# Performance work log

Measured on AMD Instinct MI355X. Metric: run time of the kernel, lower is better.

## Reference

```python
import jax, jax.numpy as jnp
import numpy as np

B, N, C = 4, 1024, 768
H = 12
HD = C // H  # 64
SCALE = HD ** -0.5


def setup_inputs() -> dict:
    key = jax.random.key(0)
    ks = jax.random.split(key, 8)
    s = lambda fan: 1.0 / np.sqrt(fan)
    return {
        "inputs": jax.random.normal(ks[0], (B, N, C), jnp.float32),
        "w_qkv": jax.random.normal(ks[1], (C, 3 * C), jnp.float32) * s(C),
        "w_l": jax.random.normal(ks[2], (H, H), jnp.float32) * s(H),
        "b_l": jnp.zeros((H,), jnp.float32),
        "w_w": jax.random.normal(ks[3], (H, H), jnp.float32) * s(H),
        "b_w": jnp.zeros((H,), jnp.float32),
        "w_proj": jax.random.normal(ks[4], (C, C), jnp.float32) * s(C),
        "b_proj": jnp.zeros((C,), jnp.float32),
    }


def reference(inputs, w_qkv, w_l, b_l, w_w, b_w, w_proj, b_proj):
    b, n, c = inputs.shape
    qkv = inputs @ w_qkv                      # (B,N,3C), no bias (use_att_bias=False)
    qkv = qkv.reshape(b, n, 3, H, HD)
    qkv = jnp.transpose(qkv, (2, 0, 3, 1, 4))  # (3,B,H,N,HD)
    q = qkv[0] * SCALE
    k = qkv[1]
    v = qkv[2]
    att = jnp.einsum("bhqd,bhkd->bhqk", q, k)            # (B,H,N,N)
    # pre-softmax talking-heads mix over head axis
    att = jnp.einsum("bhqk,hg->bgqk", att, w_l) + b_l[None, :, None, None]
    att = jax.nn.softmax(att, axis=-1)
    # post-softmax talking-heads mix
    att = jnp.einsum("bhqk,hg->bgqk", att, w_w) + b_w[None, :, None, None]
    x = jnp.einsum("bhqk,bhkd->bqhd", att, v).reshape(b, n, c)
    return x @ w_proj + b_proj
```

## Files before the change

### kernel.cpp

```cpp
#include <hip/hip_runtime.h>


#define Bsz   4
#define Nseq  1024
#define Cdim  768
#define Hn    12
#define HDim  64

typedef __attribute__((ext_vector_type(4))) float    f32x4;
typedef __attribute__((ext_vector_type(8))) _Float16 f16x8;
typedef __attribute__((ext_vector_type(4))) _Float16 f16x4;

#define MFMA_F16(A, B, C) __builtin_amdgcn_mfma_f32_16x16x32_f16(A, B, C, 0, 0, 0)

__global__ __launch_bounds__(256) void cvt_f32_f16(
    const float* __restrict__ in, _Float16* __restrict__ out)
{
  const size_t i = (size_t)(blockIdx.x * 256 + threadIdx.x) * 4;
  float4 v = *(const float4*)(in + i);
  f16x4 o;
  o[0] = (_Float16)v.x; o[1] = (_Float16)v.y;
  o[2] = (_Float16)v.z; o[3] = (_Float16)v.w;
  *(f16x4*)(out + i) = o;
}

__global__ __launch_bounds__(256) void transpose_cvt(
    const float* __restrict__ in, _Float16* __restrict__ out, int R, int C)
{
  __shared__ float T[64][65];
  const int c0 = blockIdx.x * 64, r0 = blockIdx.y * 64;
  const int lr = threadIdx.x >> 4, lc = (threadIdx.x & 15) * 4;
#pragma unroll
  for (int i = 0; i < 4; ++i) {
    float4 v = *(const float4*)(in + (size_t)(r0 + lr + i*16) * C + c0 + lc);
    T[lr+i*16][lc+0] = v.x; T[lr+i*16][lc+1] = v.y;
    T[lr+i*16][lc+2] = v.z; T[lr+i*16][lc+3] = v.w;
  }
  __syncthreads();
#pragma unroll
  for (int i = 0; i < 4; ++i) {
    const int orow = lr + i*16;
    f16x4 o;
#pragma unroll
    for (int j = 0; j < 4; ++j) o[j] = (_Float16)T[lc+j][orow];
    *(f16x4*)(out + (size_t)(c0 + orow) * R + r0 + lc) = o;
  }
}

__global__ __launch_bounds__(256, 2) void gemm_f16(
    const _Float16* __restrict__ A, const _Float16* __restrict__ Bt,
    const float* __restrict__ bias, _Float16* __restrict__ C16,
    float* __restrict__ C32, int M, int N, int K)
{
  __shared__ _Float16 sA[2][4][512];
  __shared__ _Float16 sB[2][4][512];
  const int tid = threadIdx.x;
  const int w = tid >> 6, lane = tid & 63;
  const int m0 = blockIdx.y * 128, n0 = blockIdx.x * 128;
  const int frow = lane & 15, fk8 = lane >> 4;

  f32x4 acc[4][4];
#pragma unroll
  for (int i = 0; i < 4; ++i)
#pragma unroll
    for (int j = 0; j < 4; ++j) acc[i][j] = (f32x4)0.f;

  const _Float16* gsrc = (w < 2)
      ? A  + (size_t)(m0 + w*64 + frow) * K + fk8 * 8
      : Bt + (size_t)(n0 + (w - 2)*64 + frow) * K + fk8 * 8;

  for (int kt = 0; kt < K; kt += 32) {
    f16x8 st[4];
#pragma unroll
    for (int j = 0; j < 4; ++j)
      st[j] = *(const f16x8*)(gsrc + kt + (size_t)j * 16 * K);
    __syncthreads();
    if (w < 2) {
#pragma unroll
      for (int j = 0; j < 4; ++j) *(f16x8*)&sA[w][j][lane*8] = st[j];
    } else {
#pragma unroll
      for (int j = 0; j < 4; ++j) *(f16x8*)&sB[w-2][j][lane*8] = st[j];
    }
    __syncthreads();
    f16x8 af[4], bf[4];
#pragma unroll
    for (int mi = 0; mi < 4; ++mi) af[mi] = *(const f16x8*)&sA[w & 1][mi][lane*8];
#pragma unroll
    for (int ni = 0; ni < 4; ++ni) bf[ni] = *(const f16x8*)&sB[w >> 1][ni][lane*8];
#pragma unroll
    for (int mi = 0; mi < 4; ++mi)
#pragma unroll
      for (int ni = 0; ni < 4; ++ni)
        acc[mi][ni] = MFMA_F16(af[mi], bf[ni], acc[mi][ni]);
  }

  const int m0w = m0 + (w & 1) * 64, n0w = n0 + (w >> 1) * 64;
#pragma unroll
  for (int mi = 0; mi < 4; ++mi)
#pragma unroll
    for (int ni = 0; ni < 4; ++ni) {
      const int n = n0w + ni*16 + (lane & 15);
#pragma unroll
      for (int r = 0; r < 4; ++r) {
        const int m = m0w + mi*16 + (lane >> 4)*4 + r;
        if (C16) C16[(size_t)m * N + n] = (_Float16)acc[mi][ni][r];
        else     C32[(size_t)m * N + n] = acc[mi][ni][r] + bias[n];
      }
    }
}

__global__ __launch_bounds__(256, 2) void gemm_s16(
    const _Float16* __restrict__ qkv16, _Float16* __restrict__ S)
{
  __shared__ _Float16 sA[2][4][512];
  __shared__ _Float16 sB[2][4][512];
  const int tid = threadIdx.x;
  const int w = tid >> 6, lane = tid & 63;
  const int m0 = blockIdx.y * 128, n0 = blockIdx.x * 128;
  const int frow = lane & 15, fk8 = lane >> 4;
  const int bh = blockIdx.z;
  const int b = bh / Hn, h = bh % Hn;

  const _Float16* Abase = qkv16 + (size_t)(b * Nseq) * (3*Cdim) + h * HDim;
  const _Float16* Bbase = Abase + Cdim;

  f32x4 acc[4][4];
#pragma unroll
  for (int i = 0; i < 4; ++i)
#pragma unroll
    for (int j = 0; j < 4; ++j) acc[i][j] = (f32x4)0.f;

  const _Float16* gsrc = (w < 2)
      ? Abase + (size_t)(m0 + w*64 + frow) * (3*Cdim) + fk8 * 8
      : Bbase + (size_t)(n0 + (w - 2)*64 + frow) * (3*Cdim) + fk8 * 8;

#pragma unroll
  for (int kt = 0; kt < HDim; kt += 32) {
    f16x8 st[4];
#pragma unroll
    for (int j = 0; j < 4; ++j)
      st[j] = *(const f16x8*)(gsrc + kt + (size_t)j * 16 * (3*Cdim));
    __syncthreads();
    if (w < 2) {
#pragma unroll
      for (int j = 0; j < 4; ++j) *(f16x8*)&sA[w][j][lane*8] = st[j];
    } else {
#pragma unroll
      for (int j = 0; j < 4; ++j) *(f16x8*)&sB[w-2][j][lane*8] = st[j];
    }
    __syncthreads();
    f16x8 af[4], bf[4];
#pragma unroll
    for (int mi = 0; mi < 4; ++mi) af[mi] = *(const f16x8*)&sA[w & 1][mi][lane*8];
#pragma unroll
    for (int ni = 0; ni < 4; ++ni) bf[ni] = *(const f16x8*)&sB[w >> 1][ni][lane*8];
#pragma unroll
    for (int mi = 0; mi < 4; ++mi)
#pragma unroll
      for (int ni = 0; ni < 4; ++ni)
        acc[mi][ni] = MFMA_F16(af[mi], bf[ni], acc[mi][ni]);
  }

  _Float16* out = S + ((size_t)bh << 20);
  const int m0w = m0 + (w & 1) * 64, n0w = n0 + (w >> 1) * 64;
#pragma unroll
  for (int mi = 0; mi < 4; ++mi)
#pragma unroll
    for (int ni = 0; ni < 4; ++ni) {
      const int n = n0w + ni*16 + (lane & 15);
#pragma unroll
      for (int r = 0; r < 4; ++r) {
        const int m = m0w + mi*16 + (lane >> 4)*4 + r;
        out[(size_t)m * Nseq + n] = (_Float16)acc[mi][ni][r];
      }
    }
}

__global__ __launch_bounds__(256) void mixexp_k(
    _Float16* __restrict__ S, const float* __restrict__ w_l)
{
  __shared__ __attribute__((aligned(16))) float wl_s[144];
  __shared__ float dred[4][12];
  __shared__ float dfin[2][12];
  const int tid = threadIdx.x;
  if (tid < 144) wl_s[tid] = w_l[tid] * 0.125f;
  __syncthreads();

  const int b   = blockIdx.x >> 9;
  const int qp  = blockIdx.x & 511;
  const int ql  = tid >> 7;
  const int q   = qp * 2 + ql;
  const int ks  = (tid & 127) * 8;
  _Float16* base = S + ((size_t)(b*Hn) << 20) + ((size_t)q << 10) + ks;

  f16x8 sv[12];
#pragma unroll
  for (int h = 0; h < 12; ++h) sv[h] = *(const f16x8*)(base + ((size_t)h << 20));

  float dacc[12];
#pragma unroll
  for (int g = 0; g < 12; ++g) dacc[g] = 0.f;
  f16x8 pv[12];

#pragma unroll
  for (int kk = 0; kk < 8; ++kk) {
    float L[12];
#pragma unroll
    for (int g = 0; g < 12; ++g) L[g] = 0.f;
#pragma unroll
    for (int h = 0; h < 12; ++h) {
      const float s = (float)sv[h][kk];
      const f32x4 w0 = *(const f32x4*)&wl_s[h*12];
      const f32x4 w1 = *(const f32x4*)&wl_s[h*12+4];
      const f32x4 w2 = *(const f32x4*)&wl_s[h*12+8];
#pragma unroll
      for (int j = 0; j < 4; ++j) {
        L[j]   = fmaf(s, w0[j], L[j]);
        L[4+j] = fmaf(s, w1[j], L[4+j]);
        L[8+j] = fmaf(s, w2[j], L[8+j]);
      }
    }
#pragma unroll
    for (int g = 0; g < 12; ++g) {
      const _Float16 p16 = (_Float16)__expf(L[g] - 6.0f);
      pv[g][kk] = p16;
      dacc[g] += (float)p16;
    }
  }

  const int w = tid >> 6;
#pragma unroll
  for (int g = 0; g < 12; ++g) {
    float v = dacc[g];
    v += __shfl_xor(v, 1, 64);
    v += __shfl_xor(v, 2, 64);
    v += __shfl_xor(v, 4, 64);
    v += __shfl_xor(v, 8, 64);
    v += __shfl_xor(v, 16, 64);
    v += __shfl_xor(v, 32, 64);
    dacc[g] = v;
  }
  if ((tid & 63) == 0) {
#pragma unroll
    for (int g = 0; g < 12; ++g) dred[w][g] = dacc[g];
  }
  __syncthreads();
  if (tid < 24) {
    const int qi = tid / 12, g = tid % 12;
    dfin[qi][g] = 1.0f / (dred[qi*2][g] + dred[qi*2+1][g]);
  }
  __syncthreads();

#pragma unroll
  for (int g = 0; g < 12; ++g) {
    const float df = dfin[ql][g];
    f16x8 t = pv[g];
#pragma unroll
    for (int kk = 0; kk < 8; ++kk) t[kk] = (_Float16)((float)t[kk] * df);
    *(f16x8*)(base + ((size_t)g << 20)) = t;
  }
}

__global__ __launch_bounds__(256) void prep_v(
    const _Float16* __restrict__ qkv16, _Float16* __restrict__ Vt)
{
  __shared__ float vt[64][65];
  const int id = blockIdx.x;
  const int nt = id & 15;
  const int h  = (id >> 4) % Hn;
  const int b  = id / (16 * Hn);
  const int n0 = nt * 64;
  const int tid = threadIdx.x;
  const int row = tid >> 2;
  const int c0  = (tid & 3) * 16;

  const _Float16* src = qkv16 + (size_t)(b*Nseq + n0 + row) * (3*Cdim) + 2*Cdim + h*HDim + c0;
  f16x8 v0 = *(const f16x8*)src;
  f16x8 v1 = *(const f16x8*)(src + 8);
#pragma unroll
  for (int j = 0; j < 8; ++j) {
    vt[c0+j][row]   = (float)v0[j];
    vt[c0+8+j][row] = (float)v1[j];
  }
  __syncthreads();
  f16x8 o0, o1;
#pragma unroll
  for (int j = 0; j < 8; ++j) {
    o0[j] = (_Float16)vt[row][c0+j];
    o1[j] = (_Float16)vt[row][c0+8+j];
  }
  _Float16* dst = Vt + (size_t)((b*Hn + h)*HDim + row) * Nseq + n0 + c0;
  *(f16x8*)dst = o0;
  *(f16x8*)(dst + 8) = o1;
}

__global__ __launch_bounds__(256, 3) void pvmix2_k(
    const _Float16* __restrict__ P, const _Float16* __restrict__ Vt,
    const float* __restrict__ w_w, const float* __restrict__ b_w,
    float* __restrict__ x32)
{
  __shared__ _Float16 P_s[12][16][72];
  __shared__ __attribute__((aligned(16))) float ww_s[144];
  __shared__ float bw_s[12];

  const int tid = threadIdx.x;
  const int w = tid >> 6, lane = tid & 63;
  const int col = lane & 15, grp = lane >> 4;
  const int kq = blockIdx.x & 3;
  const int qt = (blockIdx.x >> 2) & 63;
  const int b  = blockIdx.x >> 8;
  const int q0 = qt << 4;

  if (tid < 144) ww_s[tid] = w_w[tid];
  if (tid < 12)  bw_s[tid] = b_w[tid];
  __syncthreads();

  f32x4 Y[12];
#pragma unroll
  for (int g2 = 0; g2 < 12; ++g2) Y[g2] = (f32x4)0.f;

  const int kk4 = (w*4 + grp) * 4;
  const _Float16* pb0 = P + ((size_t)(b*Hn) << 20) + ((size_t)(q0 + col) << 10);

  for (int c = kq*4; c < kq*4 + 4; ++c) {
    const int k0 = c * 64;
    float pf[12][4];
#pragma unroll
    for (int g = 0; g < 12; ++g) {
      const f16x4 t = *(const f16x4*)(pb0 + ((size_t)g << 20) + k0 + kk4);
#pragma unroll
      for (int j = 0; j < 4; ++j) pf[g][j] = (float)t[j];
    }
    __syncthreads();
#pragma unroll
    for (int g2 = 0; g2 < 12; ++g2) {
      float a0 = bw_s[g2], a1 = a0, a2 = a0, a3 = a0;
#pragma unroll
      for (int g = 0; g < 12; ++g) {
        const float wv = ww_s[g*12 + g2];
        a0 = fmaf(pf[g][0], wv, a0);
        a1 = fmaf(pf[g][1], wv, a1);
        a2 = fmaf(pf[g][2], wv, a2);
        a3 = fmaf(pf[g][3], wv, a3);
      }
      f16x4 o;
      o[0] = (_Float16)a0; o[1] = (_Float16)a1;
      o[2] = (_Float16)a2; o[3] = (_Float16)a3;
      *(f16x4*)&P_s[g2][col][kk4] = o;
    }
    __syncthreads();
#pragma unroll
    for (int g2 = 0; g2 < 12; ++g2) {
      f16x8 a0 = *(const f16x8*)&P_s[g2][col][grp*8];
      f16x8 a1 = *(const f16x8*)&P_s[g2][col][32 + grp*8];
      const _Float16* vb = Vt + (size_t)((b*Hn + g2)*HDim + w*16 + col) * Nseq
                           + k0 + grp*8;
      f16x8 v0 = *(const f16x8*)vb;
      f16x8 v1 = *(const f16x8*)(vb + 32);
      Y[g2] = MFMA_F16(a0, v0, Y[g2]);
      Y[g2] = MFMA_F16(a1, v1, Y[g2]);
    }
  }

#pragma unroll
  for (int g2 = 0; g2 < 12; ++g2)
#pragma unroll
    for (int r = 0; r < 4; ++r)
      atomicAdd(&x32[(size_t)(b*Nseq + q0 + grp*4 + r) * Cdim + g2*HDim + w*16 + col],
                Y[g2][r]);
}

__global__ __launch_bounds__(256, 2) void dsum_k(
    const _Float16* __restrict__ qkv16, const float* __restrict__ w_l,
    float* __restrict__ dpart)
{
  __shared__ __attribute__((aligned(16))) float wl_s[144];
  __shared__ float dred[4][16][12];
  const int tid = threadIdx.x;
  const int w = tid >> 6, lane = tid & 63;
  const int col = lane & 15, grp = lane >> 4;
  const int ch = blockIdx.x & 7;
  const int qt = (blockIdx.x >> 3) & 63;
  const int b  = blockIdx.x >> 9;
  const int q0 = qt << 4;

  if (tid < 144) wl_s[tid] = w_l[tid] * 0.125f;

  f16x8 qf[12][2];
  {
    const _Float16* qrow = qkv16 + (size_t)(b*Nseq + q0 + col) * (3*Cdim) + grp*8;
#pragma unroll
    for (int h = 0; h < 12; ++h) {
      qf[h][0] = *(const f16x8*)(qrow + h*HDim);
      qf[h][1] = *(const f16x8*)(qrow + h*HDim + 32);
    }
  }
  __syncthreads();

  float dacc[4][12];
#pragma unroll
  for (int r = 0; r < 4; ++r)
#pragma unroll
    for (int g = 0; g < 12; ++g) dacc[r][g] = 0.f;

#pragma unroll
  for (int kg = 0; kg < 2; ++kg) {
    const int key = ch*128 + kg*64 + w*16 + col;
    const _Float16* krow = qkv16 + (size_t)(b*Nseq + key) * (3*Cdim) + Cdim + grp*8;
    f32x4 S[12];
#pragma unroll
    for (int h = 0; h < 12; ++h) {
      f16x8 b0 = *(const f16x8*)(krow + h*HDim);
      f16x8 b1 = *(const f16x8*)(krow + h*HDim + 32);
      f32x4 s = (f32x4)0.f;
      s = MFMA_F16(qf[h][0], b0, s);
      S[h] = MFMA_F16(qf[h][1], b1, s);
    }
#pragma unroll
    for (int r = 0; r < 4; ++r) {
      float L[12];
#pragma unroll
      for (int g = 0; g < 12; ++g) L[g] = 0.f;
#pragma unroll
      for (int h = 0; h < 12; ++h) {
        const float s = S[h][r];
        const f32x4 w0 = *(const f32x4*)&wl_s[h*12];
        const f32x4 w1 = *(const f32x4*)&wl_s[h*12+4];
        const f32x4 w2 = *(const f32x4*)&wl_s[h*12+8];
#pragma unroll
        for (int j = 0; j < 4; ++j) {
          L[j]   = fmaf(s, w0[j], L[j]);
          L[4+j] = fmaf(s, w1[j], L[4+j]);
          L[8+j] = fmaf(s, w2[j], L[8+j]);
        }
      }
#pragma unroll
      for (int g = 0; g < 12; ++g) dacc[r][g] += __expf(L[g] - 6.0f);
    }
  }
#pragma unroll
  for (int r = 0; r < 4; ++r)
#pragma unroll
    for (int g = 0; g < 12; ++g) {
      float v = dacc[r][g];
      v += __shfl_xor(v, 1, 64);
      v += __shfl_xor(v, 2, 64);
      v += __shfl_xor(v, 4, 64);
      v += __shfl_xor(v, 8, 64);
      dacc[r][g] = v;
    }
  if (col == 0) {
#pragma unroll
    for (int r = 0; r < 4; ++r)
#pragma unroll
      for (int g = 0; g < 12; ++g) dred[w][grp*4+r][g] = dacc[r][g];
  }
  __syncthreads();
  if (tid < 192) {
    const int q = tid / 12, g = tid % 12;
    const float s = dred[0][q][g] + dred[1][q][g] + dred[2][q][g] + dred[3][q][g];
    dpart[((size_t)((b*Hn + g)*Nseq) + q0 + q) * 8 + ch] = s;
  }
}

__global__ __launch_bounds__(256) void dinv_k(
    const float* __restrict__ dpart, float* __restrict__ dinv)
{
  const int i = blockIdx.x * 256 + threadIdx.x;
  const float* p = dpart + (size_t)i * 8;
  f32x4 a = *(const f32x4*)p;
  f32x4 c = *(const f32x4*)(p + 4);
  dinv[i] = 1.0f / (a[0]+a[1]+a[2]+a[3]+c[0]+c[1]+c[2]+c[3]);
}

__global__ __launch_bounds__(256, 2) void pvmix_k(
    const _Float16* __restrict__ qkv16, const _Float16* __restrict__ Vt,
    const float* __restrict__ dinv,
    const float* __restrict__ w_l, const float* __restrict__ w_w,
    const float* __restrict__ b_w, float* __restrict__ x32)
{
  __shared__ _Float16 P_s[12][16][72];
  __shared__ float dinv_s[16][12];
  __shared__ __attribute__((aligned(16))) float wl_s[144];
  __shared__ __attribute__((aligned(16))) float ww_s[144];
  __shared__ float bw_s[12];

  const int tid = threadIdx.x;
  const int w = tid >> 6, lane = tid & 63;
  const int col = lane & 15, grp = lane >> 4;
  const int kh = blockIdx.x & 1;
  const int qt = (blockIdx.x >> 1) & 63;
  const int b  = blockIdx.x >> 7;
  const int q0 = qt << 4;

  if (tid < 144) { wl_s[tid] = w_l[tid] * 0.125f; ww_s[tid] = w_w[tid]; }
  if (tid < 12)  bw_s[tid] = b_w[tid];
  if (tid < 192) {
    const int q = tid / 12, g = tid % 12;
    dinv_s[q][g] = dinv[(size_t)((b*Hn + g)*Nseq) + q0 + q];
  }

  f16x8 qf[12][2];
  {
    const _Float16* qrow = qkv16 + (size_t)(b*Nseq + q0 + col) * (3*Cdim) + grp*8;
#pragma unroll
    for (int h = 0; h < 12; ++h) {
      qf[h][0] = *(const f16x8*)(qrow + h*HDim);
      qf[h][1] = *(const f16x8*)(qrow + h*HDim + 32);
    }
  }
  __syncthreads();

  f32x4 Y[12];
#pragma unroll
  for (int g2 = 0; g2 < 12; ++g2) Y[g2] = (f32x4)0.f;

  for (int c = kh*8; c < kh*8 + 8; ++c) {
    const int k0 = c * 64;
    const _Float16* krow = qkv16 + (size_t)(b*Nseq + k0 + w*16 + col) * (3*Cdim)
                           + Cdim + grp*8;
    f32x4 S[12];
#pragma unroll
    for (int h = 0; h < 12; ++h) {
      f16x8 b0 = *(const f16x8*)(krow + h*HDim);
      f16x8 b1 = *(const f16x8*)(krow + h*HDim + 32);
      f32x4 s = (f32x4)0.f;
      s = MFMA_F16(qf[h][0], b0, s);
      S[h] = MFMA_F16(qf[h][1], b1, s);
    }
    __syncthreads();
#pragma unroll
    for (int r = 0; r < 4; ++r) {
      const int q = grp*4 + r;
      float L[12];
#pragma unroll
      for (int g = 0; g < 12; ++g) L[g] = 0.f;
#pragma unroll
      for (int h = 0; h < 12; ++h) {
        const float s = S[h][r];
        const f32x4 w0 = *(const f32x4*)&wl_s[h*12];
        const f32x4 w1 = *(const f32x4*)&wl_s[h*12+4];
        const f32x4 w2 = *(const f32x4*)&wl_s[h*12+8];
#pragma unroll
        for (int j = 0; j < 4; ++j) {
          L[j]   = fmaf(s, w0[j], L[j]);
          L[4+j] = fmaf(s, w1[j], L[4+j]);
          L[8+j] = fmaf(s, w2[j], L[8+j]);
        }
      }
      float att2[12];
#pragma unroll
      for (int g2 = 0; g2 < 12; ++g2) att2[g2] = bw_s[g2];
#pragma unroll
      for (int g = 0; g < 12; ++g) {
        const float pr = __expf(L[g] - 6.0f) * dinv_s[q][g];
        const f32x4 w0 = *(const f32x4*)&ww_s[g*12];
        const f32x4 w1 = *(const f32x4*)&ww_s[g*12+4];
        const f32x4 w2 = *(const f32x4*)&ww_s[g*12+8];
#pragma unroll
        for (int j = 0; j < 4; ++j) {
          att2[j]   = fmaf(pr, w0[j], att2[j]);
          att2[4+j] = fmaf(pr, w1[j], att2[4+j]);
          att2[8+j] = fmaf(pr, w2[j], att2[8+j]);
        }
      }
#pragma unroll
      for (int g2 = 0; g2 < 12; ++g2)
        P_s[g2][q][w*16 + col] = (_Float16)att2[g2];
    }
    __syncthreads();
#pragma unroll
    for (int g2 = 0; g2 < 12; ++g2) {
      f16x8 a0 = *(const f16x8*)&P_s[g2][col][grp*8];
      f16x8 a1 = *(const f16x8*)&P_s[g2][col][32 + grp*8];
      const _Float16* vb = Vt + (size_t)((b*Hn + g2)*HDim + w*16 + col) * Nseq
                           + k0 + grp*8;
      f16x8 v0 = *(const f16x8*)vb;
      f16x8 v1 = *(const f16x8*)(vb + 32);
      Y[g2] = MFMA_F16(a0, v0, Y[g2]);
      Y[g2] = MFMA_F16(a1, v1, Y[g2]);
    }
  }

#pragma unroll
  for (int g2 = 0; g2 < 12; ++g2)
#pragma unroll
    for (int r = 0; r < 4; ++r)
      atomicAdd(&x32[(size_t)(b*Nseq + q0 + grp*4 + r) * Cdim + g2*HDim + w*16 + col],
                Y[g2][r]);
}

extern "C" void kernel_launch(void* const* d_in, const int* in_sizes, int n_in,
                              void* d_out, int out_size, void* d_ws, size_t ws_size,
                              hipStream_t stream) {
  (void)in_sizes; (void)n_in; (void)out_size;
  const float* inputs = (const float*)d_in[0];
  const float* w_qkv  = (const float*)d_in[1];
  const float* w_l    = (const float*)d_in[2];
  const float* w_w    = (const float*)d_in[4];
  const float* b_w    = (const float*)d_in[5];
  const float* w_proj = (const float*)d_in[6];
  const float* b_proj = (const float*)d_in[7];
  float* out = (float*)d_out;

  const int M = Bsz * Nseq;
  char* ws = (char*)d_ws;
  _Float16* A16   = (_Float16*)ws;
  _Float16* BtQKV = A16   + (size_t)M * Cdim;
  _Float16* BtPrj = BtQKV + (size_t)(3*Cdim) * Cdim;
  _Float16* qkv16 = BtPrj + (size_t)Cdim * Cdim;
  _Float16* Vt    = qkv16 + (size_t)M * 3 * Cdim;
  _Float16* x16   = Vt    + (size_t)M * Cdim;
  float*    dpart = (float*)(x16 + (size_t)M * Cdim);
  float*    dinv  = dpart + (size_t)Bsz*Hn*Nseq*8;
  float*    x32   = dinv  + (size_t)Bsz*Hn*Nseq;
  _Float16* S     = (_Float16*)(x32 + (size_t)M * Cdim);

  const size_t NEED = 42467328ull + 14352384ull + 100663296ull;

  cvt_f32_f16<<<dim3((M * Cdim) / 1024), 256, 0, stream>>>(inputs, A16);
  transpose_cvt<<<dim3((3*Cdim)/64, Cdim/64), 256, 0, stream>>>(w_qkv, BtQKV, Cdim, 3*Cdim);
  transpose_cvt<<<dim3(Cdim/64, Cdim/64), 256, 0, stream>>>(w_proj, BtPrj, Cdim, Cdim);

  gemm_f16<<<dim3((3*Cdim)/128, M/128), 256, 0, stream>>>(
      A16, BtQKV, nullptr, qkv16, nullptr, M, 3*Cdim, Cdim);

  prep_v<<<dim3(Bsz*Hn*16), 256, 0, stream>>>(qkv16, Vt);

  if (ws_size >= NEED) {
    gemm_s16<<<dim3(Nseq/128, Nseq/128, Bsz*Hn), 256, 0, stream>>>(qkv16, S);
    mixexp_k<<<dim3(Bsz*Nseq/2), 256, 0, stream>>>(S, w_l);
    hipMemsetAsync(x32, 0, (size_t)M*Cdim*sizeof(float), stream);
    pvmix2_k<<<dim3(Bsz*64*4), 256, 0, stream>>>(S, Vt, w_w, b_w, x32);
  } else {
    dsum_k<<<dim3(Bsz*64*8), 256, 0, stream>>>(qkv16, w_l, dpart);
    dinv_k<<<dim3(Bsz*Hn*Nseq/256), 256, 0, stream>>>(dpart, dinv);
    hipMemsetAsync(x32, 0, (size_t)M*Cdim*sizeof(float), stream);
    pvmix_k<<<dim3(Bsz*64*2), 256, 0, stream>>>(
        qkv16, Vt, dinv, w_l, w_w, b_w, x32);
  }

  cvt_f32_f16<<<dim3((M * Cdim) / 1024), 256, 0, stream>>>(x32, x16);

  gemm_f16<<<dim3(Cdim/128, M/128), 256, 0, stream>>>(
      x16, BtPrj, b_proj, nullptr, out, M, Cdim, Cdim);
}
```

Measured before the change: 330.8 us.

## Fuse post-softmax head mix into exp kernel and use plain PV GEMM

The post-softmax talking-heads mix (w_w, b_w) moves into the softmax normalisation kernel, which now writes fully mixed probabilities back to S. The P·V step then becomes a plain per-head GEMM writing fp16 straight into x16. This removes the split-K fp32 atomics, the x32 memset and the fp32-to-fp16 conversion pass. In exchange the exp kernel does more ALU work per element, and the new GEMM has a small N-tile (64) that uses only three of its four waves for loads.

Measured after the change: 288.4 us. -12.8%, faster.

```diff
diff --git a/kernel.cpp b/kernel.cpp
--- a/kernel.cpp
+++ b/kernel.cpp
@@ -177,14 +177,18 @@
     }
 }
 
-__global__ __launch_bounds__(256) void mixexp_k(
-    _Float16* __restrict__ S, const float* __restrict__ w_l)
+__global__ __launch_bounds__(256) void mixexp2_k(
+    _Float16* __restrict__ S, const float* __restrict__ w_l,
+    const float* __restrict__ w_w, const float* __restrict__ b_w)
 {
   __shared__ __attribute__((aligned(16))) float wl_s[144];
+  __shared__ __attribute__((aligned(16))) float ww_s[144];
+  __shared__ float bw_s[12];
   __shared__ float dred[4][12];
   __shared__ float dfin[2][12];
   const int tid = threadIdx.x;
-  if (tid < 144) wl_s[tid] = w_l[tid] * 0.125f;
+  if (tid < 144) { wl_s[tid] = w_l[tid] * 0.125f; ww_s[tid] = w_w[tid]; }
+  if (tid < 12)  bw_s[tid] = b_w[tid];
   __syncthreads();
 
   const int b   = blockIdx.x >> 9;
@@ -252,14 +256,36 @@
   }
   __syncthreads();
 
-#pragma unroll
-  for (int g = 0; g < 12; ++g) {
-    const float df = dfin[ql][g];
-    f16x8 t = pv[g];
-#pragma unroll
-    for (int kk = 0; kk < 8; ++kk) t[kk] = (_Float16)((float)t[kk] * df);
-    *(f16x8*)(base + ((size_t)g << 20)) = t;
-  }
+  float df[12];
+#pragma unroll
+  for (int g = 0; g < 12; ++g) df[g] = dfin[ql][g];
+#pragma unroll
+  for (int kk = 0; kk < 8; ++kk) {
+    float pr[12];
+#pragma unroll
+    for (int g = 0; g < 12; ++g) pr[g] = (float)pv[g][kk] * df[g];
+    float att2[12];
+#pragma unroll
+    for (int g2 = 0; g2 < 12; ++g2) att2[g2] = bw_s[g2];
+#pragma unroll
+    for (int g = 0; g < 12; ++g) {
+      const f32x4 w0 = *(const f32x4*)&ww_s[g*12];
+      const f32x4 w1 = *(const f32x4*)&ww_s[g*12+4];
+      const f32x4 w2 = *(const f32x4*)&ww_s[g*12+8];
+#pragma unroll
+      for (int j = 0; j < 4; ++j) {
+        att2[j]   = fmaf(pr[g], w0[j], att2[j]);
+        att2[4+j] = fmaf(pr[g], w1[j], att2[4+j]);
+        att2[8+j] = fmaf(pr[g], w2[j], att2[8+j]);
+      }
+    }
+#pragma unroll
+    for (int g2 = 0; g2 < 12; ++g2) pv[g2][kk] = (_Float16)att2[g2];
+  }
+
+#pragma unroll
+  for (int g2 = 0; g2 < 12; ++g2)
+    *(f16x8*)(base + ((size_t)g2 << 20)) = pv[g2];
 }
 
 __global__ __launch_bounds__(256) void prep_v(
@@ -295,80 +321,72 @@
   *(f16x8*)(dst + 8) = o1;
 }
 
-__global__ __launch_bounds__(256, 3) void pvmix2_k(
+__global__ __launch_bounds__(256, 2) void gemm_pv(
     const _Float16* __restrict__ P, const _Float16* __restrict__ Vt,
-    const float* __restrict__ w_w, const float* __restrict__ b_w,
-    float* __restrict__ x32)
-{
-  __shared__ _Float16 P_s[12][16][72];
-  __shared__ __attribute__((aligned(16))) float ww_s[144];
-  __shared__ float bw_s[12];
-
+    _Float16* __restrict__ x16)
+{
+  __shared__ _Float16 sA[2][4][512];
+  __shared__ _Float16 sB[4][512];
   const int tid = threadIdx.x;
   const int w = tid >> 6, lane = tid & 63;
-  const int col = lane & 15, grp = lane >> 4;
-  const int kq = blockIdx.x & 3;
-  const int qt = (blockIdx.x >> 2) & 63;
-  const int b  = blockIdx.x >> 8;
-  const int q0 = qt << 4;
-
-  if (tid < 144) ww_s[tid] = w_w[tid];
-  if (tid < 12)  bw_s[tid] = b_w[tid];
-  __syncthreads();
-
-  f32x4 Y[12];
-#pragma unroll
-  for (int g2 = 0; g2 < 12; ++g2) Y[g2] = (f32x4)0.f;
-
-  const int kk4 = (w*4 + grp) * 4;
-  const _Float16* pb0 = P + ((size_t)(b*Hn) << 20) + ((size_t)(q0 + col) << 10);
-
-  for (int c = kq*4; c < kq*4 + 4; ++c) {
-    const int k0 = c * 64;
-    float pf[12][4];
-#pragma unroll
-    for (int g = 0; g < 12; ++g) {
-      const f16x4 t = *(const f16x4*)(pb0 + ((size_t)g << 20) + k0 + kk4);
-#pragma unroll
-      for (int j = 0; j < 4; ++j) pf[g][j] = (float)t[j];
-    }
-    __syncthreads();
-#pragma unroll
-    for (int g2 = 0; g2 < 12; ++g2) {
-      float a0 = bw_s[g2], a1 = a0, a2 = a0, a3 = a0;
-#pragma unroll
-      for (int g = 0; g < 12; ++g) {
-        const float wv = ww_s[g*12 + g2];
-        a0 = fmaf(pf[g][0], wv, a0);
-        a1 = fmaf(pf[g][1], wv, a1);
-        a2 = fmaf(pf[g][2], wv, a2);
-        a3 = fmaf(pf[g][3], wv, a3);
-      }
-      f16x4 o;
-      o[0] = (_Float16)a0; o[1] = (_Float16)a1;
-      o[2] = (_Float16)a2; o[3] = (_Float16)a3;
-      *(f16x4*)&P_s[g2][col][kk4] = o;
-    }
-    __syncthreads();
-#pragma unroll
-    for (int g2 = 0; g2 < 12; ++g2) {
-      f16x8 a0 = *(const f16x8*)&P_s[g2][col][grp*8];
-      f16x8 a1 = *(const f16x8*)&P_s[g2][col][32 + grp*8];
-      const _Float16* vb = Vt + (size_t)((b*Hn + g2)*HDim + w*16 + col) * Nseq
-                           + k0 + grp*8;
-      f16x8 v0 = *(const f16x8*)vb;
-      f16x8 v1 = *(const f16x8*)(vb + 32);
-      Y[g2] = MFMA_F16(a0, v0, Y[g2]);
-      Y[g2] = MFMA_F16(a1, v1, Y[g2]);
-    }
-  }
-
-#pragma unroll
-  for (int g2 = 0; g2 < 12; ++g2)
-#pragma unroll
-    for (int r = 0; r < 4; ++r)
-      atomicAdd(&x32[(size_t)(b*Nseq + q0 + grp*4 + r) * Cdim + g2*HDim + w*16 + col],
-                Y[g2][r]);
+  const int m0 = blockIdx.y * 128;
+  const int bh = blockIdx.z;
+  const int b = bh / Hn, g2 = bh % Hn;
+  const int frow = lane & 15, fk8 = lane >> 4;
+
+  const _Float16* Abase = P + ((size_t)bh << 20);
+  const _Float16* Bbase = Vt + (size_t)(bh * HDim) * Nseq;
+
+  f32x4 acc[4][2];
+#pragma unroll
+  for (int i = 0; i < 4; ++i)
+#pragma unroll
+    for (int j = 0; j < 2; ++j) acc[i][j] = (f32x4)0.f;
+
+  const _Float16* gsrc = (w < 2)
+      ? Abase + (size_t)(m0 + w*64 + frow) * Nseq + fk8 * 8
+      : Bbase + (size_t)frow * Nseq + fk8 * 8;
+
+  for (int kt = 0; kt < Nseq; kt += 32) {
+    f16x8 st[4];
+    if (w <= 2) {
+#pragma unroll
+      for (int j = 0; j < 4; ++j)
+        st[j] = *(const f16x8*)(gsrc + kt + (size_t)j * 16 * Nseq);
+    }
+    __syncthreads();
+    if (w < 2) {
+#pragma unroll
+      for (int j = 0; j < 4; ++j) *(f16x8*)&sA[w][j][lane*8] = st[j];
+    } else if (w == 2) {
+#pragma unroll
+      for (int j = 0; j < 4; ++j) *(f16x8*)&sB[j][lane*8] = st[j];
+    }
+    __syncthreads();
+    f16x8 af[4], bf[2];
+#pragma unroll
+    for (int mi = 0; mi < 4; ++mi) af[mi] = *(const f16x8*)&sA[w & 1][mi][lane*8];
+#pragma unroll
+    for (int ni = 0; ni < 2; ++ni) bf[ni] = *(const f16x8*)&sB[(w >> 1)*2 + ni][lane*8];
+#pragma unroll
+    for (int mi = 0; mi < 4; ++mi)
+#pragma unroll
+      for (int ni = 0; ni < 2; ++ni)
+        acc[mi][ni] = MFMA_F16(af[mi], bf[ni], acc[mi][ni]);
+  }
+
+  const int m0w = m0 + (w & 1) * 64, n0w = (w >> 1) * 32;
+#pragma unroll
+  for (int mi = 0; mi < 4; ++mi)
+#pragma unroll
+    for (int ni = 0; ni < 2; ++ni) {
+      const int n = n0w + ni*16 + (lane & 15);
+#pragma unroll
+      for (int r = 0; r < 4; ++r) {
+        const int m = m0w + mi*16 + (lane >> 4)*4 + r;
+        x16[(size_t)(b*Nseq + m) * Cdim + g2*HDim + n] = (_Float16)acc[mi][ni][r];
+      }
+    }
 }
 
 __global__ __launch_bounds__(256, 2) void dsum_k(
@@ -630,18 +648,16 @@
 
   if (ws_size >= NEED) {
     gemm_s16<<<dim3(Nseq/128, Nseq/128, Bsz*Hn), 256, 0, stream>>>(qkv16, S);
-    mixexp_k<<<dim3(Bsz*Nseq/2), 256, 0, stream>>>(S, w_l);
-    hipMemsetAsync(x32, 0, (size_t)M*Cdim*sizeof(float), stream);
-    pvmix2_k<<<dim3(Bsz*64*4), 256, 0, stream>>>(S, Vt, w_w, b_w, x32);
+    mixexp2_k<<<dim3(Bsz*Nseq/2), 256, 0, stream>>>(S, w_l, w_w, b_w);
+    gemm_pv<<<dim3(1, Nseq/128, Bsz*Hn), 256, 0, stream>>>(S, Vt, x16);
   } else {
     dsum_k<<<dim3(Bsz*64*8), 256, 0, stream>>>(qkv16, w_l, dpart);
     dinv_k<<<dim3(Bsz*Hn*Nseq/256), 256, 0, stream>>>(dpart, dinv);
     hipMemsetAsync(x32, 0, (size_t)M*Cdim*sizeof(float), stream);
     pvmix_k<<<dim3(Bsz*64*2), 256, 0, stream>>>(
         qkv16, Vt, dinv, w_l, w_w, b_w, x32);
-  }
-
-  cvt_f32_f16<<<dim3((M * Cdim) / 1024), 256, 0, stream>>>(x32, x16);
+    cvt_f32_f16<<<dim3((M * Cdim) / 1024), 256, 0, stream>>>(x32, x16);
+  }
 
   gemm_f16<<<dim3(Cdim/128, M/128), 256, 0, stream>>>(
       x16, BtPrj, b_proj, nullptr, out, M, Cdim, Cdim);
```
